# Kernel optimization log

Measured on AMD Instinct MI355X. Metric: run time of the kernel, lower is better.

The kernel has to match this reference:

```python
import jax, jax.numpy as jnp
import numpy as np

B, T, D_IN, H, D_OUT = 256, 512, 64, 256, 8


def setup_inputs() -> dict:
    key = jax.random.key(0)
    ks = jax.random.split(key, 6)
    s_ih = 1.0 / np.sqrt(H)
    inputs = jax.random.normal(ks[0], (B, T, D_IN), dtype=jnp.float32)
    h0 = jnp.zeros((B, H), dtype=jnp.float32)
    c0 = jnp.zeros((B, H), dtype=jnp.float32)
    # LSTM cell params, PyTorch gate order (i, f, g, o)
    W_ih = jax.random.uniform(ks[1], (4 * H, D_IN), minval=-s_ih, maxval=s_ih, dtype=jnp.float32)
    W_hh = jax.random.uniform(ks[2], (4 * H, H), minval=-s_ih, maxval=s_ih, dtype=jnp.float32)
    b = jax.random.uniform(ks[3], (4 * H,), minval=-s_ih, maxval=s_ih, dtype=jnp.float32)
    # output projection (xavier_uniform weight, zero bias)
    lim = np.sqrt(6.0 / (H + D_OUT))
    W_out = jax.random.uniform(ks[4], (D_OUT, H), minval=-lim, maxval=lim, dtype=jnp.float32)
    b_out = jnp.zeros((D_OUT,), dtype=jnp.float32)
    return {"inputs": inputs, "h0": h0, "c0": c0, "W_ih": W_ih, "W_hh": W_hh,
            "b": b, "W_out": W_out, "b_out": b_out}


def _lstm_last(inputs, h0, c0, W_ih, W_hh, b):
    # inputs: [B, T, D_in] -> scan over time, keep only final hidden state
    xs = jnp.swapaxes(inputs, 0, 1)  # [T, B, D_in]

    def step(carry, x_t):
        h, c = carry
        gates = x_t @ W_ih.T + h @ W_hh.T + b  # [B, 4H]
        i, f, g, o = jnp.split(gates, 4, axis=-1)
        c_new = jax.nn.sigmoid(f) * c + jax.nn.sigmoid(i) * jnp.tanh(g)
        h_new = jax.nn.sigmoid(o) * jnp.tanh(c_new)
        return (h_new, c_new), None

    (h, c), _ = jax.lax.scan(step, (h0, c0), xs)
    return h, c


def reference(inputs, h0, c0, W_ih, W_hh, b, W_out, b_out):
    h, c = _lstm_last(inputs, h0, c0, W_ih, W_hh, b)
    rnn_outputs = h  # last-timestep output (dropout_prob=0 -> identity)
    logits = rnn_outputs @ W_out.T + b_out
    return (rnn_outputs, logits, h, c)
```

## Files before the change

kernel.cpp:

```cpp
#include <hip/hip_runtime.h>

#define T_ 512
#define B_ 256
#define H_ 256
#define DIN_ 64

typedef __attribute__((ext_vector_type(8))) short short8;
typedef __attribute__((ext_vector_type(4))) float f32x4;
typedef __attribute__((ext_vector_type(4))) unsigned int u32x4;

__device__ __forceinline__ unsigned short f2bf(float f) {
  unsigned u = __float_as_uint(f);
  u += 0x7FFFu + ((u >> 16) & 1u);
  return (unsigned short)(u >> 16);
}
__device__ __forceinline__ float bf2f(unsigned short s) {
  return __uint_as_float(((unsigned)s) << 16);
}
__device__ __forceinline__ float sigm(float x) { return 1.0f / (1.0f + __expf(-x)); }
__device__ __forceinline__ float tanh_(float x) {
  float xx = fminf(fmaxf(x, -30.0f), 30.0f);
  float e = __expf(2.0f * xx);
  return (e - 1.0f) / (e + 1.0f);
}

__device__ __forceinline__ void load16_sc1(const unsigned* p, u32x4& a,
                                           u32x4& b, u32x4& c, u32x4& d) {
  asm volatile(
      "global_load_dwordx4 %0, %4, off sc1\n\t"
      "global_load_dwordx4 %1, %4, off offset:16 sc1\n\t"
      "global_load_dwordx4 %2, %4, off offset:32 sc1\n\t"
      "global_load_dwordx4 %3, %4, off offset:48 sc1\n\t"
      "s_waitcnt vmcnt(0)"
      : "=v"(a), "=v"(b), "=v"(c), "=v"(d)
      : "v"(p) : "memory");
}

__device__ __forceinline__ bool tags_ok(u32x4 a, u32x4 b, u32x4 c, u32x4 d,
                                        unsigned w) {
  unsigned m = (a.x >> 16) ^ w; m |= (a.y >> 16) ^ w;
  m |= (a.z >> 16) ^ w;         m |= (a.w >> 16) ^ w;
  m |= (b.x >> 16) ^ w;         m |= (b.y >> 16) ^ w;
  m |= (b.z >> 16) ^ w;         m |= (b.w >> 16) ^ w;
  m |= (c.x >> 16) ^ w;         m |= (c.y >> 16) ^ w;
  m |= (c.z >> 16) ^ w;         m |= (c.w >> 16) ^ w;
  m |= (d.x >> 16) ^ w;         m |= (d.y >> 16) ^ w;
  m |= (d.z >> 16) ^ w;         m |= (d.w >> 16) ^ w;
  return m == 0;
}

__global__ __launch_bounds__(256) void lstm_kern(
    const float* __restrict__ xin, const float* __restrict__ h0f,
    const float* __restrict__ c0f, const float* __restrict__ Wih,
    const float* __restrict__ Whh, const float* __restrict__ bias,
    const float* __restrict__ Wout, const float* __restrict__ bout,
    float* __restrict__ out, unsigned* hbuf32)
{
  const int tid = threadIdx.x;
  const int gb  = blockIdx.x >> 4;
  const int gc  = blockIdx.x & 15;
  const int wv  = tid >> 6;
  const int ln  = tid & 63;
  const int colB = ln & 15;
  const int krow = ln >> 4;

  __shared__ unsigned short h_s[2][16 * 264];
  __shared__ unsigned short x_s[2][16 * 72];

  const int gg = colB >> 2, qq = colB & 3;
  const int j = gg * H_ + gc * 16 + wv * 4 + qq;
  short8 bh[8], bx[2];
  #pragma unroll
  for (int kc = 0; kc < 8; ++kc) {
    const float* p = Whh + j * H_ + kc * 32 + krow * 8;
    short8 f;
    #pragma unroll
    for (int i = 0; i < 8; ++i) f[i] = (short)f2bf(p[i]);
    bh[kc] = f;
  }
  #pragma unroll
  for (int kc = 0; kc < 2; ++kc) {
    const float* p = Wih + j * DIN_ + kc * 32 + krow * 8;
    short8 f;
    #pragma unroll
    for (int i = 0; i < 8; ++i) f[i] = (short)f2bf(p[i]);
    bx[kc] = f;
  }
  const float bval = bias[j];

  const int quad = ln >> 4;
  const int r_lo = (ln >> 2) & 3;
  const int q    = ln & 3;
  const int erow = quad * 4 + r_lo;
  const int grow = gb * 16 + erow;
  const int gcol = gc * 16 + wv * 4 + q;
  float c_val = c0f[grow * H_ + gcol];
  float h_val = 0.0f;

  const int hr = tid >> 4;
  const int hcb = (tid & 15) * 16;
  const unsigned* ldp_base = hbuf32 + gb * 4096 + hr * 256 + hcb;
  unsigned* stp_base = hbuf32 + gb * 4096 + erow * 256 + gcol;

  const float* xrow = xin + ((gb * 16 + (tid >> 4)) * T_) * DIN_ + (tid & 15) * 4;

  for (int s = 1; s <= T_; ++s) {
    const int p = (s - 1) & 1;
    {
      float4 v = *(const float4*)(xrow + (s - 1) * DIN_);
      unsigned short* qp = &x_s[p][(tid >> 4) * 72 + (tid & 15) * 4];
      qp[0] = f2bf(v.x); qp[1] = f2bf(v.y); qp[2] = f2bf(v.z); qp[3] = f2bf(v.w);
    }
    if (s == 1) {
      #pragma unroll
      for (int it = 0; it < 4; ++it) {
        int e4 = tid + it * 256;
        int r = e4 >> 6, c4 = e4 & 63;
        float4 v = *((const float4*)(h0f + (gb * 16 + r) * H_) + c4);
        unsigned short* qp = &h_s[p][r * 264 + c4 * 4];
        qp[0] = f2bf(v.x); qp[1] = f2bf(v.y); qp[2] = f2bf(v.z); qp[3] = f2bf(v.w);
      }
    } else {
      const unsigned want = (unsigned)(s - 1);
      const unsigned* ldp = ldp_base + (((s - 1) & 1) << 16);
      u32x4 va, vb, vc, vd;
      int tries = 0;
      do {
        load16_sc1(ldp, va, vb, vc, vd);
        if (tags_ok(va, vb, vc, vd, want)) break;
      } while (++tries < (1 << 18));
      unsigned* q32 = (unsigned*)&h_s[p][hr * 264 + hcb];
      q32[0] = (va.x & 0xFFFFu) | (va.y << 16);
      q32[1] = (va.z & 0xFFFFu) | (va.w << 16);
      q32[2] = (vb.x & 0xFFFFu) | (vb.y << 16);
      q32[3] = (vb.z & 0xFFFFu) | (vb.w << 16);
      q32[4] = (vc.x & 0xFFFFu) | (vc.y << 16);
      q32[5] = (vc.z & 0xFFFFu) | (vc.w << 16);
      q32[6] = (vd.x & 0xFFFFu) | (vd.y << 16);
      q32[7] = (vd.z & 0xFFFFu) | (vd.w << 16);
    }
    __syncthreads();

    f32x4 acc = {0.f, 0.f, 0.f, 0.f};
    #pragma unroll
    for (int kc = 0; kc < 2; ++kc) {
      short8 a = *(const short8*)&x_s[p][colB * 72 + kc * 32 + krow * 8];
      acc = __builtin_amdgcn_mfma_f32_16x16x32_bf16(a, bx[kc], acc, 0, 0, 0);
    }
    #pragma unroll
    for (int kc = 0; kc < 8; ++kc) {
      short8 a = *(const short8*)&h_s[p][colB * 264 + kc * 32 + krow * 8];
      acc = __builtin_amdgcn_mfma_f32_16x16x32_bf16(a, bh[kc], acc, 0, 0, 0);
    }

    float v0 = acc[0] + bval, v1 = acc[1] + bval,
          v2 = acc[2] + bval, v3 = acc[3] + bval;
    {
      int g0 = (ln >> 2) & 1;
      float s0 = g0 ? v0 : v1, s1 = g0 ? v2 : v3;
      float t0 = __shfl_xor(s0, 4, 64), t1 = __shfl_xor(s1, 4, 64);
      if (g0) { v0 = t0; v2 = t1; } else { v1 = t0; v3 = t1; }
    }
    {
      int g1 = (ln >> 3) & 1;
      float s0 = g1 ? v0 : v2, s1 = g1 ? v1 : v3;
      float t0 = __shfl_xor(s0, 8, 64), t1 = __shfl_xor(s1, 8, 64);
      if (g1) { v0 = t0; v1 = t1; } else { v2 = t0; v3 = t1; }
    }

    c_val = sigm(v1) * c_val + sigm(v0) * tanh_(v2);
    h_val = sigm(v3) * tanh_(c_val);
    unsigned pk = ((unsigned)s << 16) | (unsigned)f2bf(h_val);
    __hip_atomic_store(stp_base + ((s & 1) << 16), pk,
                       __ATOMIC_RELAXED, __HIP_MEMORY_SCOPE_AGENT);
  }

  out[grow * H_ + gcol] = h_val;
  out[67584 + grow * H_ + gcol] = h_val;
  out[133120 + grow * H_ + gcol] = c_val;

  if (gc == 0) {
    const unsigned want = (unsigned)T_;
    const unsigned* ldp = ldp_base + ((T_ & 1) << 16);
    u32x4 va, vb, vc, vd;
    int tries = 0;
    do {
      load16_sc1(ldp, va, vb, vc, vd);
      if (tags_ok(va, vb, vc, vd, want)) break;
    } while (++tries < (1 << 18));
    unsigned* q32 = (unsigned*)&h_s[0][hr * 264 + hcb];
    q32[0] = (va.x & 0xFFFFu) | (va.y << 16);
    q32[1] = (va.z & 0xFFFFu) | (va.w << 16);
    q32[2] = (vb.x & 0xFFFFu) | (vb.y << 16);
    q32[3] = (vb.z & 0xFFFFu) | (vb.w << 16);
    q32[4] = (vc.x & 0xFFFFu) | (vc.y << 16);
    q32[5] = (vc.z & 0xFFFFu) | (vc.w << 16);
    q32[6] = (vd.x & 0xFFFFu) | (vd.y << 16);
    q32[7] = (vd.z & 0xFFFFu) | (vd.w << 16);
    __syncthreads();
    if (tid < 128) {
      int r = tid >> 3, o = tid & 7;
      float a = bout[o];
      for (int k = 0; k < H_; ++k)
        a = fmaf(bf2f(h_s[0][r * 264 + k]), Wout[o * H_ + k], a);
      out[65536 + (gb * 16 + r) * 8 + o] = a;
    }
  }
}

extern "C" void kernel_launch(void* const* d_in, const int* in_sizes, int n_in,
                              void* d_out, int out_size, void* d_ws, size_t ws_size,
                              hipStream_t stream) {
  const float* xin  = (const float*)d_in[0];
  const float* h0f  = (const float*)d_in[1];
  const float* c0f  = (const float*)d_in[2];
  const float* Wih  = (const float*)d_in[3];
  const float* Whh  = (const float*)d_in[4];
  const float* bias = (const float*)d_in[5];
  const float* Wout = (const float*)d_in[6];
  const float* bout = (const float*)d_in[7];
  float* out = (float*)d_out;

  unsigned* hbuf32 = (unsigned*)d_ws;

  void* args[] = {&xin, &h0f, &c0f, &Wih, &Whh, &bias, &Wout, &bout,
                  &out, &hbuf32};
  hipLaunchCooperativeKernel((void*)lstm_kern, dim3(256), dim3(256),
                             args, 0, stream);
}
```

Measured before the change: 1.214 ms.

## Give each block four column tiles to cut grid size and cross-block sync

Each block now computes 64 hidden columns, four MFMA tiles per wave, instead of 16. The grid shrinks from 256 to 64 blocks, so only 4 blocks per batch group exchange h through global memory each step. This lowers the number of spinning participants and the polling traffic. In exchange each block does four times the MFMA and gate work per step and holds four times the weight registers, which may hurt occupancy. The cooperative launch is also replaced with a plain launch, which relies on all 64 blocks being co-resident.

```diff
diff --git a/kernel.cpp b/kernel.cpp
--- a/kernel.cpp
+++ b/kernel.cpp
@@ -57,8 +57,8 @@
     float* __restrict__ out, unsigned* hbuf32)
 {
   const int tid = threadIdx.x;
-  const int gb  = blockIdx.x >> 4;
-  const int gc  = blockIdx.x & 15;
+  const int gb  = blockIdx.x >> 2;
+  const int gc  = blockIdx.x & 3;
   const int wv  = tid >> 6;
   const int ln  = tid & 63;
   const int colB = ln & 15;
@@ -68,39 +68,52 @@
   __shared__ unsigned short x_s[2][16 * 72];
 
   const int gg = colB >> 2, qq = colB & 3;
-  const int j = gg * H_ + gc * 16 + wv * 4 + qq;
-  short8 bh[8], bx[2];
+  short8 bh[4][8], bx[4][2];
+  float bval[4];
   #pragma unroll
-  for (int kc = 0; kc < 8; ++kc) {
-    const float* p = Whh + j * H_ + kc * 32 + krow * 8;
-    short8 f;
-    #pragma unroll
-    for (int i = 0; i < 8; ++i) f[i] = (short)f2bf(p[i]);
-    bh[kc] = f;
-  }
-  #pragma unroll
-  for (int kc = 0; kc < 2; ++kc) {
-    const float* p = Wih + j * DIN_ + kc * 32 + krow * 8;
-    short8 f;
-    #pragma unroll
-    for (int i = 0; i < 8; ++i) f[i] = (short)f2bf(p[i]);
-    bx[kc] = f;
-  }
-  const float bval = bias[j];
+  for (int t = 0; t < 4; ++t) {
+    const int j = gg * H_ + gc * 64 + wv * 16 + t * 4 + qq;
+    #pragma unroll
+    for (int kc = 0; kc < 8; ++kc) {
+      const float* p = Whh + j * H_ + kc * 32 + krow * 8;
+      float4 v0 = *(const float4*)(p);
+      float4 v1 = *(const float4*)(p + 4);
+      short8 f;
+      f[0] = (short)f2bf(v0.x); f[1] = (short)f2bf(v0.y);
+      f[2] = (short)f2bf(v0.z); f[3] = (short)f2bf(v0.w);
+      f[4] = (short)f2bf(v1.x); f[5] = (short)f2bf(v1.y);
+      f[6] = (short)f2bf(v1.z); f[7] = (short)f2bf(v1.w);
+      bh[t][kc] = f;
+    }
+    #pragma unroll
+    for (int kc = 0; kc < 2; ++kc) {
+      const float* p = Wih + j * DIN_ + kc * 32 + krow * 8;
+      float4 v0 = *(const float4*)(p);
+      float4 v1 = *(const float4*)(p + 4);
+      short8 f;
+      f[0] = (short)f2bf(v0.x); f[1] = (short)f2bf(v0.y);
+      f[2] = (short)f2bf(v0.z); f[3] = (short)f2bf(v0.w);
+      f[4] = (short)f2bf(v1.x); f[5] = (short)f2bf(v1.y);
+      f[6] = (short)f2bf(v1.z); f[7] = (short)f2bf(v1.w);
+      bx[t][kc] = f;
+    }
+    bval[t] = bias[j];
+  }
 
   const int quad = ln >> 4;
   const int r_lo = (ln >> 2) & 3;
   const int q    = ln & 3;
   const int erow = quad * 4 + r_lo;
   const int grow = gb * 16 + erow;
-  const int gcol = gc * 16 + wv * 4 + q;
-  float c_val = c0f[grow * H_ + gcol];
-  float h_val = 0.0f;
+  const int cb   = gc * 64 + wv * 16 + q;
+  float c_val[4], h_val[4];
+  #pragma unroll
+  for (int t = 0; t < 4; ++t) { c_val[t] = c0f[grow * H_ + cb + t * 4]; h_val[t] = 0.f; }
 
   const int hr = tid >> 4;
   const int hcb = (tid & 15) * 16;
   const unsigned* ldp_base = hbuf32 + gb * 4096 + hr * 256 + hcb;
-  unsigned* stp_base = hbuf32 + gb * 4096 + erow * 256 + gcol;
+  unsigned* stp_base = hbuf32 + gb * 4096 + erow * 256 + cb;
 
   const float* xrow = xin + ((gb * 16 + (tid >> 4)) * T_) * DIN_ + (tid & 15) * 4;
 
@@ -141,43 +154,56 @@
     }
     __syncthreads();
 
-    f32x4 acc = {0.f, 0.f, 0.f, 0.f};
+    f32x4 acc[4];
+    #pragma unroll
+    for (int t = 0; t < 4; ++t) acc[t] = (f32x4){0.f, 0.f, 0.f, 0.f};
     #pragma unroll
     for (int kc = 0; kc < 2; ++kc) {
       short8 a = *(const short8*)&x_s[p][colB * 72 + kc * 32 + krow * 8];
-      acc = __builtin_amdgcn_mfma_f32_16x16x32_bf16(a, bx[kc], acc, 0, 0, 0);
+      #pragma unroll
+      for (int t = 0; t < 4; ++t)
+        acc[t] = __builtin_amdgcn_mfma_f32_16x16x32_bf16(a, bx[t][kc], acc[t], 0, 0, 0);
     }
     #pragma unroll
     for (int kc = 0; kc < 8; ++kc) {
       short8 a = *(const short8*)&h_s[p][colB * 264 + kc * 32 + krow * 8];
-      acc = __builtin_amdgcn_mfma_f32_16x16x32_bf16(a, bh[kc], acc, 0, 0, 0);
-    }
-
-    float v0 = acc[0] + bval, v1 = acc[1] + bval,
-          v2 = acc[2] + bval, v3 = acc[3] + bval;
-    {
-      int g0 = (ln >> 2) & 1;
-      float s0 = g0 ? v0 : v1, s1 = g0 ? v2 : v3;
-      float t0 = __shfl_xor(s0, 4, 64), t1 = __shfl_xor(s1, 4, 64);
-      if (g0) { v0 = t0; v2 = t1; } else { v1 = t0; v3 = t1; }
-    }
-    {
-      int g1 = (ln >> 3) & 1;
-      float s0 = g1 ? v0 : v2, s1 = g1 ? v1 : v3;
-      float t0 = __shfl_xor(s0, 8, 64), t1 = __shfl_xor(s1, 8, 64);
-      if (g1) { v0 = t0; v1 = t1; } else { v2 = t0; v3 = t1; }
-    }
-
-    c_val = sigm(v1) * c_val + sigm(v0) * tanh_(v2);
-    h_val = sigm(v3) * tanh_(c_val);
-    unsigned pk = ((unsigned)s << 16) | (unsigned)f2bf(h_val);
-    __hip_atomic_store(stp_base + ((s & 1) << 16), pk,
-                       __ATOMIC_RELAXED, __HIP_MEMORY_SCOPE_AGENT);
-  }
-
-  out[grow * H_ + gcol] = h_val;
-  out[67584 + grow * H_ + gcol] = h_val;
-  out[133120 + grow * H_ + gcol] = c_val;
+      #pragma unroll
+      for (int t = 0; t < 4; ++t)
+        acc[t] = __builtin_amdgcn_mfma_f32_16x16x32_bf16(a, bh[t][kc], acc[t], 0, 0, 0);
+    }
+
+    const unsigned pkhi = (unsigned)s << 16;
+    unsigned* stp = stp_base + ((s & 1) << 16);
+    #pragma unroll
+    for (int t = 0; t < 4; ++t) {
+      float v0 = acc[t][0] + bval[t], v1 = acc[t][1] + bval[t],
+            v2 = acc[t][2] + bval[t], v3 = acc[t][3] + bval[t];
+      {
+        int g0 = (ln >> 2) & 1;
+        float s0 = g0 ? v0 : v1, s1 = g0 ? v2 : v3;
+        float t0 = __shfl_xor(s0, 4, 64), t1 = __shfl_xor(s1, 4, 64);
+        if (g0) { v0 = t0; v2 = t1; } else { v1 = t0; v3 = t1; }
+      }
+      {
+        int g1 = (ln >> 3) & 1;
+        float s0 = g1 ? v0 : v2, s1 = g1 ? v1 : v3;
+        float t0 = __shfl_xor(s0, 8, 64), t1 = __shfl_xor(s1, 8, 64);
+        if (g1) { v0 = t0; v1 = t1; } else { v2 = t0; v3 = t1; }
+      }
+      c_val[t] = sigm(v1) * c_val[t] + sigm(v0) * tanh_(v2);
+      h_val[t] = sigm(v3) * tanh_(c_val[t]);
+      __hip_atomic_store(stp + t * 4, pkhi | (unsigned)f2bf(h_val[t]),
+                         __ATOMIC_RELAXED, __HIP_MEMORY_SCOPE_AGENT);
+    }
+  }
+
+  #pragma unroll
+  for (int t = 0; t < 4; ++t) {
+    const int gj = cb + t * 4;
+    out[grow * H_ + gj] = h_val[t];
+    out[67584 + grow * H_ + gj] = h_val[t];
+    out[133120 + grow * H_ + gj] = c_val[t];
+  }
 
   if (gc == 0) {
     const unsigned want = (unsigned)T_;
@@ -223,8 +249,6 @@
 
   unsigned* hbuf32 = (unsigned*)d_ws;
 
-  void* args[] = {&xin, &h0f, &c0f, &Wih, &Whh, &bias, &Wout, &bout,
-                  &out, &hbuf32};
-  hipLaunchCooperativeKernel((void*)lstm_kern, dim3(256), dim3(256),
-                             args, 0, stream);
-}
+  lstm_kern<<<dim3(64), dim3(256), 0, stream>>>(
+      xin, h0f, c0f, Wih, Whh, bias, Wout, bout, out, hbuf32);
+}
```

After: 1.541 ms. 26.9% more time.
